# Optimization experiments

Hardware: AMD Instinct MI355X
Metric: run time of the kernel (lower is better)

The kernel has to match this reference:

```python
import jax, jax.numpy as jnp
import numpy as np
from jax import lax

C = 256      # in_c == out_c == dim
NH = 8       # num_heads
K = 7        # depthwise pos-enc kernel
H1 = 512     # int(mlp_ratio * in_c) = 2.0 * 256
B, Hs, Ws = 2, 48, 48


def setup_inputs() -> dict:
    key = jax.random.key(0)
    ks = jax.random.split(key, 8)
    w = lambda k, shape: jax.random.normal(k, shape, jnp.float32) * 0.02
    return {
        "x": jax.random.normal(ks[0], (B, C, Hs, Ws), jnp.float32),
        # 1x1 convs stored as [out, in] (BN folded into weight+bias)
        "qk_w": w(ks[1], (2 * C, C)), "qk_b": jnp.zeros((2 * C,), jnp.float32),
        "v_w": w(ks[2], (C, C)),       "v_b": jnp.zeros((C,), jnp.float32),
        # depthwise positional encoding conv [C,1,K,K]
        "pe_w": w(ks[3], (C, 1, K, K)), "pe_b": jnp.zeros((C,), jnp.float32),
        "proj_w": w(ks[4], (C, C)),    "proj_b": jnp.zeros((C,), jnp.float32),
        # conv FFN: 1x1 (SiLU) -> 1x1 (no act)
        "fc1_w": w(ks[5], (H1, C)),    "fc1_b": jnp.zeros((H1,), jnp.float32),
        "fc2_w": w(ks[6], (C, H1)),    "fc2_b": jnp.zeros((C,), jnp.float32),
    }


def _c1(x, w, b):
    # 1x1 conv == per-pixel matmul
    return jnp.einsum('bchw,oc->bohw', x, w) + b[None, :, None, None]


def reference(x, qk_w, qk_b, v_w, v_b, pe_w, pe_b, proj_w, proj_b,
              fc1_w, fc1_b, fc2_w, fc2_b):
    Bb, Cc, Hh, Ww = x.shape
    hd = Cc // NH                 # head_dim = 32
    N = Hh * Ww
    scale = hd ** -0.5

    # ---- AttentionV2 ----
    qk = _c1(x, qk_w, qk_b).reshape(Bb, NH, 2 * hd, N)
    q, k = qk[:, :, :hd], qk[:, :, hd:]
    v_full = _c1(x, v_w, v_b)                      # [B,C,H,W]
    pe = lax.conv_general_dilated(
        v_full, pe_w, (1, 1), 'SAME', feature_group_count=Cc,
        dimension_numbers=('NCHW', 'OIHW', 'NCHW')) + pe_b[None, :, None, None]
    v = v_full.reshape(Bb, NH, hd, N)

    # attn = q^T @ k * scale ; softmax over keys
    attn = jax.nn.softmax(jnp.einsum('bhdn,bhdm->bhnm', q, k) * scale, axis=-1)
    o = jnp.einsum('bhdm,bhnm->bhdn', v, attn).reshape(Bb, Cc, Hh, Ww)
    attn_out = _c1(o + pe, proj_w, proj_b)

    # ---- block residuals + conv FFN (add=True) ----
    x1 = x + attn_out
    h = jax.nn.silu(_c1(x1, fc1_w, fc1_b))         # Conv(in_c, hidden, 1, 1) with SiLU
    return x1 + _c1(h, fc2_w, fc2_b)               # Conv(hidden, out_c, 1, act=False)
```

## Files before the change

### kernel.cpp

```cpp
#include <hip/hip_runtime.h>
#include <hip/hip_bf16.h>

#define NCH 256
#define NHD 8
#define HD 32
#define NPIX 2304
#define H1DIM 512

typedef __attribute__((ext_vector_type(8))) __bf16 bf16x8;
typedef __attribute__((ext_vector_type(4))) float f32x4;

__global__ __launch_bounds__(256) void prep_k(
    const float* __restrict__ x,
    const float* __restrict__ w0, const float* __restrict__ w1,
    const float* __restrict__ w2, const float* __restrict__ w3,
    const float* __restrict__ w4,
    __bf16* __restrict__ Xb, __bf16* __restrict__ Wall) {
    const int tid = threadIdx.x;
    if (blockIdx.x < 288) {
        const int t = blockIdx.x;
        const int b = t / 144, r0 = t % 144;
        const int c0 = (r0 / 36) * 64, n0 = (r0 % 36) * 64;
        __shared__ float tile[64][65];
        const size_t sb = ((size_t)b * NCH + c0) * NPIX + n0;
#pragma unroll
        for (int i = 0; i < 16; ++i) {
            int idx = tid + i * 256;
            int rr = idx >> 6, cc = idx & 63;
            tile[rr][cc] = x[sb + (size_t)rr * NPIX + cc];
        }
        __syncthreads();
#pragma unroll
        for (int i = 0; i < 8; ++i) {
            int idx = tid + i * 256;
            int nn = idx >> 5, cp = (idx & 31) * 2;
            union { __bf16 h[2]; unsigned u; } pk;
            pk.h[0] = (__bf16)tile[cp][nn];
            pk.h[1] = (__bf16)tile[cp + 1][nn];
            *(unsigned*)&Xb[((size_t)b * NPIX + n0 + nn) * NCH + c0 + cp] = pk.u;
        }
    } else {
        int i = (blockIdx.x - 288) * 256 + tid;
        const float* src; int off;
        if (i < 32768)      { src = w0; off = i; }
        else if (i < 49152) { src = w1; off = i - 32768; }
        else if (i < 65536) { src = w2; off = i - 49152; }
        else if (i < 98304) { src = w3; off = i - 65536; }
        else                { src = w4; off = i - 98304; }
        float4 v = ((const float4*)src)[off];
        union { __bf16 h[4]; uint2 u; } pk;
        pk.h[0] = (__bf16)v.x; pk.h[1] = (__bf16)v.y;
        pk.h[2] = (__bf16)v.z; pk.h[3] = (__bf16)v.w;
        ((uint2*)Wall)[i] = pk.u;
    }
}

__global__ __launch_bounds__(256) void qkv_k(
    const __bf16* __restrict__ A, const __bf16* __restrict__ Wq,
    const __bf16* __restrict__ Wv, const float* __restrict__ qk_b,
    const float* __restrict__ v_b, __bf16* __restrict__ Qb,
    __bf16* __restrict__ Kf, float* __restrict__ v_bu,
    __bf16* __restrict__ Vf) {
    const int tid = threadIdx.x;
    const int wave = tid >> 6, lane = tid & 63;
    const int l16 = lane & 15, quad = lane >> 4;
    const int h = blockIdx.x & 7;
    const int u = blockIdx.x >> 3;
    const int tau = u * 4 + wave;
    const int px = tau % 144;
    const int rest = tau / 144;
    const int b = rest & 1;
    const int sub = rest >> 1;
    const int m0 = px * 16;
    const bool isv = sub >= 4;
    const int oc0 = isv ? (32 * h + 16 * (sub - 4)) : (64 * h + 16 * sub);
    const __bf16* W = isv ? Wv : Wq;

    const __bf16* aptr = A + ((size_t)b * NPIX + m0 + l16) * NCH + quad * 8;
    const __bf16* bptr = W + (size_t)(oc0 + l16) * NCH + quad * 8;

    f32x4 acc = {0.f, 0.f, 0.f, 0.f};
#pragma unroll 8
    for (int k = 0; k < NCH; k += 32) {
        bf16x8 af = *(const bf16x8*)(aptr + k);
        bf16x8 bf = *(const bf16x8*)(bptr + k);
        acc = __builtin_amdgcn_mfma_f32_16x16x32_bf16(af, bf, acc, 0, 0, 0);
    }

    const int oc = oc0 + l16;
    const int mb = m0 + quad * 4;

    if (!isv) {
        const float bb = qk_b[oc];
        const int bh = b * NHD + h;
        const int dd = (oc0 & 16) + l16;
        if ((oc0 & 32) == 0) {
            const float qs = 0.17677669529663689f * 1.4426950408889634f;
#pragma unroll
            for (int r = 0; r < 4; ++r)
                Qb[((size_t)bh * NPIX + mb + r) * 32 + dd] = (__bf16)((acc[r] + bb) * qs);
        } else {
            __bf16* kp = Kf + ((size_t)(bh * 144 + px) * 64 + (dd >> 3) * 16 + quad * 4) * 8 + (dd & 7);
#pragma unroll
            for (int r = 0; r < 4; ++r) kp[r * 8] = (__bf16)(acc[r] + bb);
        }
    } else {
        const float bb = v_b[oc];
        const int bh = b * NHD + h;
        const int half = (oc0 >> 4) & 1;
        const size_t fb = ((size_t)b * NCH + oc) * NPIX + mb;
        float4 vf_; float* vp = &vf_.x;
        union { __bf16 hh[4]; uint2 u; } pk;
#pragma unroll
        for (int r = 0; r < 4; ++r) {
            float v = acc[r] + bb;
            vp[r] = v; pk.hh[r] = (__bf16)v;
        }
        *(float4*)&v_bu[fb] = vf_;
        *(uint2*)&Vf[((size_t)(bh * 144 + px) * 64 + lane) * 8 + half * 4] = pk.u;
    }
}

template <int IC, int OC, int OCQ, int MODE>
__global__ __launch_bounds__(256) void convmm_k(
    const __bf16* __restrict__ A, const __bf16* __restrict__ W,
    const float* __restrict__ bias, const float* __restrict__ resid,
    float* __restrict__ out_f, __bf16* __restrict__ out_b) {
    const int tid = threadIdx.x;
    const int wave = tid >> 6, lane = tid & 63;
    const int l16 = lane & 15, quad = lane >> 4;
    const int xcd = blockIdx.x & 7;
    const int u = blockIdx.x >> 3;
    const int ocq = u % OCQ;
    const int rest = u / OCQ;
    const int m8 = rest % 18;
    const int b = rest / 18;
    const int m0 = (m8 * 8 + xcd) * 16;
    const int oc0 = (ocq * 4 + wave) * 16;

    const __bf16* aptr = A + ((size_t)b * NPIX + m0 + l16) * IC + quad * 8;
    const __bf16* bptr = W + (size_t)(oc0 + l16) * IC + quad * 8;

    f32x4 acc = {0.f, 0.f, 0.f, 0.f};
#pragma unroll 8
    for (int k = 0; k < IC; k += 32) {
        bf16x8 af = *(const bf16x8*)(aptr + k);
        bf16x8 bf = *(const bf16x8*)(bptr + k);
        acc = __builtin_amdgcn_mfma_f32_16x16x32_bf16(af, bf, acc, 0, 0, 0);
    }

    const int oc = oc0 + l16;
    const int mb = m0 + quad * 4;
    const float bb = bias[oc];

    if constexpr (MODE == 2) {
        const size_t fb = ((size_t)b * OC + oc) * NPIX + mb;
        float4 xr = *(const float4*)&resid[fb];
        const float* xp = &xr.x;
        float4 vf_; float* vp = &vf_.x;
#pragma unroll
        for (int r = 0; r < 4; ++r) {
            float v = acc[r] + bb + xp[r];
            vp[r] = v;
            out_b[((size_t)b * NPIX + mb + r) * OC + oc] = (__bf16)v;
        }
        *(float4*)&out_f[fb] = vf_;
    } else if constexpr (MODE == 3) {
#pragma unroll
        for (int r = 0; r < 4; ++r) {
            float v = acc[r] + bb;
            v = v / (1.f + __expf(-v));
            out_b[((size_t)b * NPIX + mb + r) * OC + oc] = (__bf16)v;
        }
    } else {
        const size_t fb = ((size_t)b * OC + oc) * NPIX + mb;
        float4 xr = *(const float4*)&resid[fb];
        const float* xp = &xr.x;
        float4 vf_; float* vp = &vf_.x;
#pragma unroll
        for (int r = 0; r < 4; ++r) vp[r] = acc[r] + bb + xp[r];
        *(float4*)&out_f[fb] = vf_;
    }
}

__global__ __launch_bounds__(256) void dwconv_k(const float* __restrict__ vb,
                                                const float* __restrict__ pw,
                                                const float* __restrict__ pb,
                                                float* __restrict__ pe) {
    const int tid = threadIdx.x;
    const int r = (int)blockIdx.x >> 3;
    const int c = (blockIdx.x & 7) * 32 + (r & 31);
    const int b = r >> 5;
    __shared__ float plane[NPIX];
    __shared__ float wk[49];
    const size_t base = ((size_t)b * NCH + c) * NPIX;
    for (int i = tid; i < NPIX; i += 256) plane[i] = vb[base + i];
    if (tid < 49) wk[tid] = pw[c * 49 + tid];
    float bb = pb[c];
    __syncthreads();
    for (int p = tid; p < NPIX; p += 256) {
        int y = p / 48, x = p - y * 48;
        float s = bb;
#pragma unroll
        for (int ky = 0; ky < 7; ++ky) {
            int yy = y + ky - 3;
            if ((unsigned)yy < 48u) {
#pragma unroll
                for (int kx = 0; kx < 7; ++kx) {
                    int xx = x + kx - 3;
                    if ((unsigned)xx < 48u) s += wk[ky * 7 + kx] * plane[yy * 48 + xx];
                }
            }
        }
        pe[base + p] = s;
    }
}

__global__ __launch_bounds__(512) void attn6_k(const __bf16* __restrict__ Qb,
                                               const __bf16* __restrict__ Kf,
                                               const __bf16* __restrict__ Vf,
                                               const float* __restrict__ pe,
                                               __bf16* __restrict__ opb) {
    const int tid = threadIdx.x;
    const int wave = tid >> 6, lane = tid & 63;
    const int l16 = lane & 15, quad = lane >> 4;
    const int h = blockIdx.x & 7;
    const int r0 = (int)blockIdx.x >> 3;
    const int qt = r0 % 72;
    const int b = r0 / 72;
    const int qb = qt * 32;
    const int bh = b * NHD + h;

    __shared__ float o_s[8][32][33];
    __shared__ float l_s[8][32];

    bf16x8 b_q0 = *(const bf16x8*)(Qb + ((size_t)bh * NPIX + qb + l16) * 32 + quad * 8);
    bf16x8 b_q1 = *(const bf16x8*)(Qb + ((size_t)bh * NPIX + qb + 16 + l16) * 32 + quad * 8);

    const __bf16* kf = Kf + ((size_t)(bh * 144 + wave * 18) * 64 + lane) * 8;
    const __bf16* vf = Vf + ((size_t)(bh * 144 + wave * 18) * 64 + lane) * 8;

    f32x4 o00 = {0.f,0.f,0.f,0.f}, o01 = {0.f,0.f,0.f,0.f};
    f32x4 o10 = {0.f,0.f,0.f,0.f}, o11 = {0.f,0.f,0.f,0.f};
    f32x4 l0 = {0.f,0.f,0.f,0.f}, l1 = {0.f,0.f,0.f,0.f};

#pragma unroll 3
    for (int t = 0; t < 18; ++t) {
        bf16x8 a_k = *(const bf16x8*)(kf + (size_t)t * 512);
        bf16x8 va  = *(const bf16x8*)(vf + (size_t)t * 512);
        f32x4 z = {0.f, 0.f, 0.f, 0.f};
        f32x4 s0 = __builtin_amdgcn_mfma_f32_16x16x32_bf16(a_k, b_q0, z, 0, 0, 0);
        f32x4 s1 = __builtin_amdgcn_mfma_f32_16x16x32_bf16(a_k, b_q1, z, 0, 0, 0);
        f32x4 p0, p1;
#pragma unroll
        for (int r = 0; r < 4; ++r) {
            p0[r] = __builtin_amdgcn_exp2f(s0[r]);
            p1[r] = __builtin_amdgcn_exp2f(s1[r]);
        }
        l0 += p0; l1 += p1;
        bf16x8 b0lo = {}, b0hi = {}, b1lo = {}, b1hi = {};
#pragma unroll
        for (int r = 0; r < 4; ++r) {
            __bf16 c0 = (__bf16)p0[r], c1 = (__bf16)p1[r];
            b0lo[r] = c0; b0hi[4 + r] = c0;
            b1lo[r] = c1; b1hi[4 + r] = c1;
        }
        o00 = __builtin_amdgcn_mfma_f32_16x16x32_bf16(va, b0lo, o00, 0, 0, 0);
        o01 = __builtin_amdgcn_mfma_f32_16x16x32_bf16(va, b0hi, o01, 0, 0, 0);
        o10 = __builtin_amdgcn_mfma_f32_16x16x32_bf16(va, b1lo, o10, 0, 0, 0);
        o11 = __builtin_amdgcn_mfma_f32_16x16x32_bf16(va, b1hi, o11, 0, 0, 0);
    }

    float ls0 = l0[0] + l0[1] + l0[2] + l0[3];
    ls0 += __shfl_xor(ls0, 16); ls0 += __shfl_xor(ls0, 32);
    float ls1 = l1[0] + l1[1] + l1[2] + l1[3];
    ls1 += __shfl_xor(ls1, 16); ls1 += __shfl_xor(ls1, 32);

#pragma unroll
    for (int r = 0; r < 4; ++r) {
        o_s[wave][quad * 4 + r][l16]           = o00[r];
        o_s[wave][16 + quad * 4 + r][l16]      = o01[r];
        o_s[wave][quad * 4 + r][16 + l16]      = o10[r];
        o_s[wave][16 + quad * 4 + r][16 + l16] = o11[r];
    }
    if (quad == 0) { l_s[wave][l16] = ls0; l_s[wave][16 + l16] = ls1; }
    __syncthreads();

    const int q = tid & 31;
    const int d0 = (tid >> 5) * 2;
    float l = 0.f;
#pragma unroll
    for (int w = 0; w < 8; ++w) l += l_s[w][q];
    const float inv = 1.f / l;
    float v0 = 0.f, v1 = 0.f;
#pragma unroll
    for (int w = 0; w < 8; ++w) {
        v0 += o_s[w][d0][q];
        v1 += o_s[w][d0 + 1][q];
    }
    const int n = qb + q;
    const int ch = h * HD + d0;
    v0 = v0 * inv + pe[((size_t)b * NCH + ch) * NPIX + n];
    v1 = v1 * inv + pe[((size_t)b * NCH + ch + 1) * NPIX + n];
    union { __bf16 hh[2]; unsigned u; } pk;
    pk.hh[0] = (__bf16)v0; pk.hh[1] = (__bf16)v1;
    *(unsigned*)&opb[((size_t)b * NPIX + n) * NCH + ch] = pk.u;
}

extern "C" void kernel_launch(void* const* d_in, const int* in_sizes, int n_in,
                              void* d_out, int out_size, void* d_ws, size_t ws_size,
                              hipStream_t stream) {
    const float* x    = (const float*)d_in[0];
    const float* qk_w = (const float*)d_in[1];
    const float* qk_b = (const float*)d_in[2];
    const float* v_w  = (const float*)d_in[3];
    const float* v_b  = (const float*)d_in[4];
    const float* pe_w = (const float*)d_in[5];
    const float* pe_b = (const float*)d_in[6];
    const float* pj_w = (const float*)d_in[7];
    const float* pj_b = (const float*)d_in[8];
    const float* f1_w = (const float*)d_in[9];
    const float* f1_b = (const float*)d_in[10];
    const float* f2_w = (const float*)d_in[11];
    const float* f2_b = (const float*)d_in[12];
    float* out = (float*)d_out;

    const int B = 2;
    const size_t plane = (size_t)NCH * NPIX;
    const size_t bp = (size_t)B * plane;

    float* v_bu  = (float*)d_ws;
    float* pe_bu = v_bu + bp;
    float* x1_f  = pe_bu + bp;
    __bf16* Xb   = (__bf16*)(x1_f + bp);
    __bf16* opb  = Xb + bp;
    __bf16* x1b  = opb + bp;
    __bf16* hb   = x1b + bp;
    __bf16* Qb   = hb + 2 * bp;
    __bf16* Kf   = Qb + bp;
    __bf16* Vf   = Kf + bp;
    __bf16* Wall = Vf + bp;
    __bf16* Wq = Wall;
    __bf16* Wv = Wall + 131072;
    __bf16* Wp = Wall + 196608;
    __bf16* W1 = Wall + 262144;
    __bf16* W2 = Wall + 393216;

    prep_k<<<800, 256, 0, stream>>>(x, qk_w, v_w, pj_w, f1_w, f2_w, Xb, Wall);
    qkv_k<<<3456, 256, 0, stream>>>(Xb, Wq, Wv, qk_b, v_b, Qb, Kf, v_bu, Vf);
    dwconv_k<<<512, 256, 0, stream>>>(v_bu, pe_w, pe_b, pe_bu);
    attn6_k<<<1152, 512, 0, stream>>>(Qb, Kf, Vf, pe_bu, opb);
    convmm_k<256, 256, 4, 2><<<1152, 256, 0, stream>>>(opb, Wp, pj_b, x, x1_f, x1b);
    convmm_k<256, 512, 8, 3><<<2304, 256, 0, stream>>>(x1b, W1, f1_b, nullptr, nullptr, hb);
    convmm_k<512, 256, 4, 4><<<1152, 256, 0, stream>>>(hb, W2, f2_b, x1_f, out, nullptr);
}
```

Measured before the change: 208.3 us.

## Fuse all seven stages into one persistent cooperative kernel with grid syncs

Replaces the seven separate kernel launches (prep, qkv, dwconv, attention, three 1x1 convs) with a single persistent cooperative kernel. Blocks loop over each stage's tasks and are separated by grid.sync barriers. The grid size comes from an occupancy query capped at 1024 blocks. This removes per-launch overhead and inter-kernel gaps, but adds grid-wide barrier costs. Occupancy may also drop because of the larger union shared memory and register pressure across all stages.

```diff
diff --git a/kernel.cpp b/kernel.cpp
--- a/kernel.cpp
+++ b/kernel.cpp
@@ -1,142 +1,41 @@
 #include <hip/hip_runtime.h>
 #include <hip/hip_bf16.h>
+#include <hip/hip_cooperative_groups.h>
+
+namespace cg = cooperative_groups;
 
 #define NCH 256
 #define NHD 8
 #define HD 32
 #define NPIX 2304
 #define H1DIM 512
+#define NCU 256
 
 typedef __attribute__((ext_vector_type(8))) __bf16 bf16x8;
 typedef __attribute__((ext_vector_type(4))) float f32x4;
 
-__global__ __launch_bounds__(256) void prep_k(
-    const float* __restrict__ x,
-    const float* __restrict__ w0, const float* __restrict__ w1,
-    const float* __restrict__ w2, const float* __restrict__ w3,
-    const float* __restrict__ w4,
-    __bf16* __restrict__ Xb, __bf16* __restrict__ Wall) {
-    const int tid = threadIdx.x;
-    if (blockIdx.x < 288) {
-        const int t = blockIdx.x;
-        const int b = t / 144, r0 = t % 144;
-        const int c0 = (r0 / 36) * 64, n0 = (r0 % 36) * 64;
-        __shared__ float tile[64][65];
-        const size_t sb = ((size_t)b * NCH + c0) * NPIX + n0;
-#pragma unroll
-        for (int i = 0; i < 16; ++i) {
-            int idx = tid + i * 256;
-            int rr = idx >> 6, cc = idx & 63;
-            tile[rr][cc] = x[sb + (size_t)rr * NPIX + cc];
-        }
-        __syncthreads();
-#pragma unroll
-        for (int i = 0; i < 8; ++i) {
-            int idx = tid + i * 256;
-            int nn = idx >> 5, cp = (idx & 31) * 2;
-            union { __bf16 h[2]; unsigned u; } pk;
-            pk.h[0] = (__bf16)tile[cp][nn];
-            pk.h[1] = (__bf16)tile[cp + 1][nn];
-            *(unsigned*)&Xb[((size_t)b * NPIX + n0 + nn) * NCH + c0 + cp] = pk.u;
-        }
-    } else {
-        int i = (blockIdx.x - 288) * 256 + tid;
-        const float* src; int off;
-        if (i < 32768)      { src = w0; off = i; }
-        else if (i < 49152) { src = w1; off = i - 32768; }
-        else if (i < 65536) { src = w2; off = i - 49152; }
-        else if (i < 98304) { src = w3; off = i - 65536; }
-        else                { src = w4; off = i - 98304; }
-        float4 v = ((const float4*)src)[off];
-        union { __bf16 h[4]; uint2 u; } pk;
-        pk.h[0] = (__bf16)v.x; pk.h[1] = (__bf16)v.y;
-        pk.h[2] = (__bf16)v.z; pk.h[3] = (__bf16)v.w;
-        ((uint2*)Wall)[i] = pk.u;
-    }
-}
-
-__global__ __launch_bounds__(256) void qkv_k(
-    const __bf16* __restrict__ A, const __bf16* __restrict__ Wq,
-    const __bf16* __restrict__ Wv, const float* __restrict__ qk_b,
-    const float* __restrict__ v_b, __bf16* __restrict__ Qb,
-    __bf16* __restrict__ Kf, float* __restrict__ v_bu,
-    __bf16* __restrict__ Vf) {
-    const int tid = threadIdx.x;
-    const int wave = tid >> 6, lane = tid & 63;
-    const int l16 = lane & 15, quad = lane >> 4;
-    const int h = blockIdx.x & 7;
-    const int u = blockIdx.x >> 3;
-    const int tau = u * 4 + wave;
-    const int px = tau % 144;
-    const int rest = tau / 144;
-    const int b = rest & 1;
-    const int sub = rest >> 1;
-    const int m0 = px * 16;
-    const bool isv = sub >= 4;
-    const int oc0 = isv ? (32 * h + 16 * (sub - 4)) : (64 * h + 16 * sub);
-    const __bf16* W = isv ? Wv : Wq;
-
-    const __bf16* aptr = A + ((size_t)b * NPIX + m0 + l16) * NCH + quad * 8;
-    const __bf16* bptr = W + (size_t)(oc0 + l16) * NCH + quad * 8;
-
-    f32x4 acc = {0.f, 0.f, 0.f, 0.f};
-#pragma unroll 8
-    for (int k = 0; k < NCH; k += 32) {
-        bf16x8 af = *(const bf16x8*)(aptr + k);
-        bf16x8 bf = *(const bf16x8*)(bptr + k);
-        acc = __builtin_amdgcn_mfma_f32_16x16x32_bf16(af, bf, acc, 0, 0, 0);
-    }
-
-    const int oc = oc0 + l16;
-    const int mb = m0 + quad * 4;
-
-    if (!isv) {
-        const float bb = qk_b[oc];
-        const int bh = b * NHD + h;
-        const int dd = (oc0 & 16) + l16;
-        if ((oc0 & 32) == 0) {
-            const float qs = 0.17677669529663689f * 1.4426950408889634f;
-#pragma unroll
-            for (int r = 0; r < 4; ++r)
-                Qb[((size_t)bh * NPIX + mb + r) * 32 + dd] = (__bf16)((acc[r] + bb) * qs);
-        } else {
-            __bf16* kp = Kf + ((size_t)(bh * 144 + px) * 64 + (dd >> 3) * 16 + quad * 4) * 8 + (dd & 7);
-#pragma unroll
-            for (int r = 0; r < 4; ++r) kp[r * 8] = (__bf16)(acc[r] + bb);
-        }
-    } else {
-        const float bb = v_b[oc];
-        const int bh = b * NHD + h;
-        const int half = (oc0 >> 4) & 1;
-        const size_t fb = ((size_t)b * NCH + oc) * NPIX + mb;
-        float4 vf_; float* vp = &vf_.x;
-        union { __bf16 hh[4]; uint2 u; } pk;
-#pragma unroll
-        for (int r = 0; r < 4; ++r) {
-            float v = acc[r] + bb;
-            vp[r] = v; pk.hh[r] = (__bf16)v;
-        }
-        *(float4*)&v_bu[fb] = vf_;
-        *(uint2*)&Vf[((size_t)(bh * 144 + px) * 64 + lane) * 8 + half * 4] = pk.u;
-    }
-}
+union SMem {
+    float tile[64][65];
+    struct { float plane[NPIX]; float wk[64]; } dw;
+    struct { float o[8][32][33]; float l[8][32]; } at;
+};
 
 template <int IC, int OC, int OCQ, int MODE>
-__global__ __launch_bounds__(256) void convmm_k(
-    const __bf16* __restrict__ A, const __bf16* __restrict__ W,
+__device__ __forceinline__ void convmm_task(
+    int T, const __bf16* __restrict__ A, const __bf16* __restrict__ W,
     const float* __restrict__ bias, const float* __restrict__ resid,
-    float* __restrict__ out_f, __bf16* __restrict__ out_b) {
-    const int tid = threadIdx.x;
-    const int wave = tid >> 6, lane = tid & 63;
-    const int l16 = lane & 15, quad = lane >> 4;
-    const int xcd = blockIdx.x & 7;
-    const int u = blockIdx.x >> 3;
+    float* __restrict__ out_f, __bf16* __restrict__ out_b,
+    int l16, int quad) {
+    const int w4 = T & 3;
+    const int obid = T >> 2;
+    const int xcd = obid & 7;
+    const int u = obid >> 3;
     const int ocq = u % OCQ;
     const int rest = u / OCQ;
     const int m8 = rest % 18;
     const int b = rest / 18;
     const int m0 = (m8 * 8 + xcd) * 16;
-    const int oc0 = (ocq * 4 + wave) * 16;
+    const int oc0 = (ocq * 4 + w4) * 16;
 
     const __bf16* aptr = A + ((size_t)b * NPIX + m0 + l16) * IC + quad * 8;
     const __bf16* bptr = W + (size_t)(oc0 + l16) * IC + quad * 8;
@@ -183,128 +82,250 @@
     }
 }
 
-__global__ __launch_bounds__(256) void dwconv_k(const float* __restrict__ vb,
-                                                const float* __restrict__ pw,
-                                                const float* __restrict__ pb,
-                                                float* __restrict__ pe) {
-    const int tid = threadIdx.x;
-    const int r = (int)blockIdx.x >> 3;
-    const int c = (blockIdx.x & 7) * 32 + (r & 31);
-    const int b = r >> 5;
-    __shared__ float plane[NPIX];
-    __shared__ float wk[49];
-    const size_t base = ((size_t)b * NCH + c) * NPIX;
-    for (int i = tid; i < NPIX; i += 256) plane[i] = vb[base + i];
-    if (tid < 49) wk[tid] = pw[c * 49 + tid];
-    float bb = pb[c];
-    __syncthreads();
-    for (int p = tid; p < NPIX; p += 256) {
-        int y = p / 48, x = p - y * 48;
-        float s = bb;
-#pragma unroll
-        for (int ky = 0; ky < 7; ++ky) {
-            int yy = y + ky - 3;
-            if ((unsigned)yy < 48u) {
-#pragma unroll
-                for (int kx = 0; kx < 7; ++kx) {
-                    int xx = x + kx - 3;
-                    if ((unsigned)xx < 48u) s += wk[ky * 7 + kx] * plane[yy * 48 + xx];
-                }
-            }
-        }
-        pe[base + p] = s;
-    }
-}
-
-__global__ __launch_bounds__(512) void attn6_k(const __bf16* __restrict__ Qb,
-                                               const __bf16* __restrict__ Kf,
-                                               const __bf16* __restrict__ Vf,
-                                               const float* __restrict__ pe,
-                                               __bf16* __restrict__ opb) {
+__global__ __launch_bounds__(512, 4) void fused_k(
+    const float* __restrict__ x, const float* __restrict__ qk_w,
+    const float* __restrict__ v_w, const float* __restrict__ pj_w,
+    const float* __restrict__ f1_w, const float* __restrict__ f2_w,
+    const float* __restrict__ qk_b, const float* __restrict__ v_b,
+    const float* __restrict__ pe_w, const float* __restrict__ pe_b,
+    const float* __restrict__ pj_b, const float* __restrict__ f1_b,
+    const float* __restrict__ f2_b,
+    float* __restrict__ out, float* __restrict__ v_bu,
+    float* __restrict__ pe_bu, float* __restrict__ x1_f,
+    __bf16* __restrict__ Xb, __bf16* __restrict__ opb,
+    __bf16* __restrict__ x1b, __bf16* __restrict__ hb,
+    __bf16* __restrict__ Qb, __bf16* __restrict__ Kf,
+    __bf16* __restrict__ Vf, __bf16* __restrict__ Wall) {
+    cg::grid_group grid = cg::this_grid();
     const int tid = threadIdx.x;
     const int wave = tid >> 6, lane = tid & 63;
     const int l16 = lane & 15, quad = lane >> 4;
-    const int h = blockIdx.x & 7;
-    const int r0 = (int)blockIdx.x >> 3;
-    const int qt = r0 % 72;
-    const int b = r0 / 72;
-    const int qb = qt * 32;
-    const int bh = b * NHD + h;
-
-    __shared__ float o_s[8][32][33];
-    __shared__ float l_s[8][32];
-
-    bf16x8 b_q0 = *(const bf16x8*)(Qb + ((size_t)bh * NPIX + qb + l16) * 32 + quad * 8);
-    bf16x8 b_q1 = *(const bf16x8*)(Qb + ((size_t)bh * NPIX + qb + 16 + l16) * 32 + quad * 8);
-
-    const __bf16* kf = Kf + ((size_t)(bh * 144 + wave * 18) * 64 + lane) * 8;
-    const __bf16* vf = Vf + ((size_t)(bh * 144 + wave * 18) * 64 + lane) * 8;
-
-    f32x4 o00 = {0.f,0.f,0.f,0.f}, o01 = {0.f,0.f,0.f,0.f};
-    f32x4 o10 = {0.f,0.f,0.f,0.f}, o11 = {0.f,0.f,0.f,0.f};
-    f32x4 l0 = {0.f,0.f,0.f,0.f}, l1 = {0.f,0.f,0.f,0.f};
+    const int bid = (int)blockIdx.x;
+    const int nb = (int)gridDim.x;
+
+    __shared__ SMem sm;
+
+    const __bf16* Wq = Wall;
+    const __bf16* Wv = Wall + 131072;
+    const __bf16* Wp = Wall + 196608;
+    const __bf16* W1 = Wall + 262144;
+    const __bf16* W2 = Wall + 393216;
+
+    for (int t = bid; t < 288; t += nb) {
+        const int b = t / 144, r0 = t % 144;
+        const int c0 = (r0 / 36) * 64, n0 = (r0 % 36) * 64;
+        const size_t sb = ((size_t)b * NCH + c0) * NPIX + n0;
+        for (int i = tid; i < 4096; i += 512) {
+            int rr = i >> 6, cc = i & 63;
+            sm.tile[rr][cc] = x[sb + (size_t)rr * NPIX + cc];
+        }
+        __syncthreads();
+        for (int i = tid; i < 2048; i += 512) {
+            int nn = i >> 5, cp = (i & 31) * 2;
+            union { __bf16 h[2]; unsigned u; } pk;
+            pk.h[0] = (__bf16)sm.tile[cp][nn];
+            pk.h[1] = (__bf16)sm.tile[cp + 1][nn];
+            *(unsigned*)&Xb[((size_t)b * NPIX + n0 + nn) * NCH + c0 + cp] = pk.u;
+        }
+        __syncthreads();
+    }
+    for (int i = bid * 512 + tid; i < 131072; i += nb * 512) {
+        const float* src; int off;
+        if (i < 32768)      { src = qk_w; off = i; }
+        else if (i < 49152) { src = v_w;  off = i - 32768; }
+        else if (i < 65536) { src = pj_w; off = i - 49152; }
+        else if (i < 98304) { src = f1_w; off = i - 65536; }
+        else                { src = f2_w; off = i - 98304; }
+        float4 v = ((const float4*)src)[off];
+        union { __bf16 h[4]; uint2 u; } pk;
+        pk.h[0] = (__bf16)v.x; pk.h[1] = (__bf16)v.y;
+        pk.h[2] = (__bf16)v.z; pk.h[3] = (__bf16)v.w;
+        ((uint2*)Wall)[i] = pk.u;
+    }
+    grid.sync();
+
+    {
+        const int h = bid & 7;
+        const int slots = (nb >> 3) * 8;
+        for (int tau = (bid >> 3) * 8 + wave; tau < 1728; tau += slots) {
+            const int px = tau % 144;
+            const int rest = tau / 144;
+            const int b = rest & 1;
+            const int sub = rest >> 1;
+            const int m0 = px * 16;
+            const bool isv = sub >= 4;
+            const int oc0 = isv ? (32 * h + 16 * (sub - 4)) : (64 * h + 16 * sub);
+            const __bf16* W = isv ? Wv : Wq;
+
+            const __bf16* aptr = Xb + ((size_t)b * NPIX + m0 + l16) * NCH + quad * 8;
+            const __bf16* bptr = W + (size_t)(oc0 + l16) * NCH + quad * 8;
+
+            f32x4 acc = {0.f, 0.f, 0.f, 0.f};
+#pragma unroll 8
+            for (int k = 0; k < NCH; k += 32) {
+                bf16x8 af = *(const bf16x8*)(aptr + k);
+                bf16x8 bf = *(const bf16x8*)(bptr + k);
+                acc = __builtin_amdgcn_mfma_f32_16x16x32_bf16(af, bf, acc, 0, 0, 0);
+            }
+
+            const int oc = oc0 + l16;
+            const int mb = m0 + quad * 4;
+
+            if (!isv) {
+                const float bb = qk_b[oc];
+                const int bh = b * NHD + h;
+                const int dd = (oc0 & 16) + l16;
+                if ((oc0 & 32) == 0) {
+                    const float qs = 0.17677669529663689f * 1.4426950408889634f;
+#pragma unroll
+                    for (int r = 0; r < 4; ++r)
+                        Qb[((size_t)bh * NPIX + mb + r) * 32 + dd] = (__bf16)((acc[r] + bb) * qs);
+                } else {
+                    __bf16* kp = Kf + ((size_t)(bh * 144 + px) * 64 + (dd >> 3) * 16 + quad * 4) * 8 + (dd & 7);
+#pragma unroll
+                    for (int r = 0; r < 4; ++r) kp[r * 8] = (__bf16)(acc[r] + bb);
+                }
+            } else {
+                const float bb = v_b[oc];
+                const int bh = b * NHD + h;
+                const int half = (oc0 >> 4) & 1;
+                const size_t fb = ((size_t)b * NCH + oc) * NPIX + mb;
+                float4 vf_; float* vp = &vf_.x;
+                union { __bf16 hh[4]; uint2 u; } pk;
+#pragma unroll
+                for (int r = 0; r < 4; ++r) {
+                    float v = acc[r] + bb;
+                    vp[r] = v; pk.hh[r] = (__bf16)v;
+                }
+                *(float4*)&v_bu[fb] = vf_;
+                *(uint2*)&Vf[((size_t)(bh * 144 + px) * 64 + lane) * 8 + half * 4] = pk.u;
+            }
+        }
+    }
+    grid.sync();
+
+    for (int t = bid; t < 512; t += nb) {
+        const int r = t >> 3;
+        const int c = (t & 7) * 32 + (r & 31);
+        const int b = r >> 5;
+        const size_t base = ((size_t)b * NCH + c) * NPIX;
+        for (int i = tid; i < NPIX; i += 512) sm.dw.plane[i] = v_bu[base + i];
+        if (tid < 49) sm.dw.wk[tid] = pe_w[c * 49 + tid];
+        const float bb = pe_b[c];
+        __syncthreads();
+        for (int p = tid; p < NPIX; p += 512) {
+            int y = p / 48, xx0 = p - y * 48;
+            float s = bb;
+#pragma unroll
+            for (int ky = 0; ky < 7; ++ky) {
+                int yy = y + ky - 3;
+                if ((unsigned)yy < 48u) {
+#pragma unroll
+                    for (int kx = 0; kx < 7; ++kx) {
+                        int xx = xx0 + kx - 3;
+                        if ((unsigned)xx < 48u) s += sm.dw.wk[ky * 7 + kx] * sm.dw.plane[yy * 48 + xx];
+                    }
+                }
+            }
+            pe_bu[base + p] = s;
+        }
+        __syncthreads();
+    }
+    grid.sync();
+
+    for (int task = bid; task < 1152; task += nb) {
+        const int h = task & 7;
+        const int r0 = task >> 3;
+        const int qt = r0 % 72;
+        const int b = r0 / 72;
+        const int qb = qt * 32;
+        const int bh = b * NHD + h;
+
+        bf16x8 b_q0 = *(const bf16x8*)(Qb + ((size_t)bh * NPIX + qb + l16) * 32 + quad * 8);
+        bf16x8 b_q1 = *(const bf16x8*)(Qb + ((size_t)bh * NPIX + qb + 16 + l16) * 32 + quad * 8);
+
+        const __bf16* kf = Kf + ((size_t)(bh * 144 + wave * 18) * 64 + lane) * 8;
+        const __bf16* vf = Vf + ((size_t)(bh * 144 + wave * 18) * 64 + lane) * 8;
+
+        f32x4 o00 = {0.f,0.f,0.f,0.f}, o01 = {0.f,0.f,0.f,0.f};
+        f32x4 o10 = {0.f,0.f,0.f,0.f}, o11 = {0.f,0.f,0.f,0.f};
+        f32x4 l0 = {0.f,0.f,0.f,0.f}, l1 = {0.f,0.f,0.f,0.f};
 
 #pragma unroll 3
-    for (int t = 0; t < 18; ++t) {
-        bf16x8 a_k = *(const bf16x8*)(kf + (size_t)t * 512);
-        bf16x8 va  = *(const bf16x8*)(vf + (size_t)t * 512);
-        f32x4 z = {0.f, 0.f, 0.f, 0.f};
-        f32x4 s0 = __builtin_amdgcn_mfma_f32_16x16x32_bf16(a_k, b_q0, z, 0, 0, 0);
-        f32x4 s1 = __builtin_amdgcn_mfma_f32_16x16x32_bf16(a_k, b_q1, z, 0, 0, 0);
-        f32x4 p0, p1;
+        for (int t = 0; t < 18; ++t) {
+            bf16x8 a_k = *(const bf16x8*)(kf + (size_t)t * 512);
+            bf16x8 va  = *(const bf16x8*)(vf + (size_t)t * 512);
+            f32x4 z = {0.f, 0.f, 0.f, 0.f};
+            f32x4 s0 = __builtin_amdgcn_mfma_f32_16x16x32_bf16(a_k, b_q0, z, 0, 0, 0);
+            f32x4 s1 = __builtin_amdgcn_mfma_f32_16x16x32_bf16(a_k, b_q1, z, 0, 0, 0);
+            f32x4 p0, p1;
+#pragma unroll
+            for (int r = 0; r < 4; ++r) {
+                p0[r] = __builtin_amdgcn_exp2f(s0[r]);
+                p1[r] = __builtin_amdgcn_exp2f(s1[r]);
+            }
+            l0 += p0; l1 += p1;
+            bf16x8 b0lo = {}, b0hi = {}, b1lo = {}, b1hi = {};
+#pragma unroll
+            for (int r = 0; r < 4; ++r) {
+                __bf16 c0 = (__bf16)p0[r], c1 = (__bf16)p1[r];
+                b0lo[r] = c0; b0hi[4 + r] = c0;
+                b1lo[r] = c1; b1hi[4 + r] = c1;
+            }
+            o00 = __builtin_amdgcn_mfma_f32_16x16x32_bf16(va, b0lo, o00, 0, 0, 0);
+            o01 = __builtin_amdgcn_mfma_f32_16x16x32_bf16(va, b0hi, o01, 0, 0, 0);
+            o10 = __builtin_amdgcn_mfma_f32_16x16x32_bf16(va, b1lo, o10, 0, 0, 0);
+            o11 = __builtin_amdgcn_mfma_f32_16x16x32_bf16(va, b1hi, o11, 0, 0, 0);
+        }
+
+        float ls0 = l0[0] + l0[1] + l0[2] + l0[3];
+        ls0 += __shfl_xor(ls0, 16); ls0 += __shfl_xor(ls0, 32);
+        float ls1 = l1[0] + l1[1] + l1[2] + l1[3];
+        ls1 += __shfl_xor(ls1, 16); ls1 += __shfl_xor(ls1, 32);
+
 #pragma unroll
         for (int r = 0; r < 4; ++r) {
-            p0[r] = __builtin_amdgcn_exp2f(s0[r]);
-            p1[r] = __builtin_amdgcn_exp2f(s1[r]);
-        }
-        l0 += p0; l1 += p1;
-        bf16x8 b0lo = {}, b0hi = {}, b1lo = {}, b1hi = {};
-#pragma unroll
-        for (int r = 0; r < 4; ++r) {
-            __bf16 c0 = (__bf16)p0[r], c1 = (__bf16)p1[r];
-            b0lo[r] = c0; b0hi[4 + r] = c0;
-            b1lo[r] = c1; b1hi[4 + r] = c1;
-        }
-        o00 = __builtin_amdgcn_mfma_f32_16x16x32_bf16(va, b0lo, o00, 0, 0, 0);
-        o01 = __builtin_amdgcn_mfma_f32_16x16x32_bf16(va, b0hi, o01, 0, 0, 0);
-        o10 = __builtin_amdgcn_mfma_f32_16x16x32_bf16(va, b1lo, o10, 0, 0, 0);
-        o11 = __builtin_amdgcn_mfma_f32_16x16x32_bf16(va, b1hi, o11, 0, 0, 0);
-    }
-
-    float ls0 = l0[0] + l0[1] + l0[2] + l0[3];
-    ls0 += __shfl_xor(ls0, 16); ls0 += __shfl_xor(ls0, 32);
-    float ls1 = l1[0] + l1[1] + l1[2] + l1[3];
-    ls1 += __shfl_xor(ls1, 16); ls1 += __shfl_xor(ls1, 32);
-
-#pragma unroll
-    for (int r = 0; r < 4; ++r) {
-        o_s[wave][quad * 4 + r][l16]           = o00[r];
-        o_s[wave][16 + quad * 4 + r][l16]      = o01[r];
-        o_s[wave][quad * 4 + r][16 + l16]      = o10[r];
-        o_s[wave][16 + quad * 4 + r][16 + l16] = o11[r];
-    }
-    if (quad == 0) { l_s[wave][l16] = ls0; l_s[wave][16 + l16] = ls1; }
-    __syncthreads();
-
-    const int q = tid & 31;
-    const int d0 = (tid >> 5) * 2;
-    float l = 0.f;
-#pragma unroll
-    for (int w = 0; w < 8; ++w) l += l_s[w][q];
-    const float inv = 1.f / l;
-    float v0 = 0.f, v1 = 0.f;
-#pragma unroll
-    for (int w = 0; w < 8; ++w) {
-        v0 += o_s[w][d0][q];
-        v1 += o_s[w][d0 + 1][q];
-    }
-    const int n = qb + q;
-    const int ch = h * HD + d0;
-    v0 = v0 * inv + pe[((size_t)b * NCH + ch) * NPIX + n];
-    v1 = v1 * inv + pe[((size_t)b * NCH + ch + 1) * NPIX + n];
-    union { __bf16 hh[2]; unsigned u; } pk;
-    pk.hh[0] = (__bf16)v0; pk.hh[1] = (__bf16)v1;
-    *(unsigned*)&opb[((size_t)b * NPIX + n) * NCH + ch] = pk.u;
+            sm.at.o[wave][quad * 4 + r][l16]           = o00[r];
+            sm.at.o[wave][16 + quad * 4 + r][l16]      = o01[r];
+            sm.at.o[wave][quad * 4 + r][16 + l16]      = o10[r];
+            sm.at.o[wave][16 + quad * 4 + r][16 + l16] = o11[r];
+        }
+        if (quad == 0) { sm.at.l[wave][l16] = ls0; sm.at.l[wave][16 + l16] = ls1; }
+        __syncthreads();
+
+        const int q = tid & 31;
+        const int d0 = (tid >> 5) * 2;
+        float l = 0.f;
+#pragma unroll
+        for (int w = 0; w < 8; ++w) l += sm.at.l[w][q];
+        const float inv = 1.f / l;
+        float v0 = 0.f, v1 = 0.f;
+#pragma unroll
+        for (int w = 0; w < 8; ++w) {
+            v0 += sm.at.o[w][d0][q];
+            v1 += sm.at.o[w][d0 + 1][q];
+        }
+        const int n = qb + q;
+        const int ch = h * HD + d0;
+        v0 = v0 * inv + pe_bu[((size_t)b * NCH + ch) * NPIX + n];
+        v1 = v1 * inv + pe_bu[((size_t)b * NCH + ch + 1) * NPIX + n];
+        union { __bf16 hh[2]; unsigned u; } pk;
+        pk.hh[0] = (__bf16)v0; pk.hh[1] = (__bf16)v1;
+        *(unsigned*)&opb[((size_t)b * NPIX + n) * NCH + ch] = pk.u;
+        __syncthreads();
+    }
+    grid.sync();
+
+    for (int T = bid * 8 + wave; T < 4608; T += nb * 8)
+        convmm_task<256, 256, 4, 2>(T, opb, Wp, pj_b, x, x1_f, x1b, l16, quad);
+    grid.sync();
+
+    for (int T = bid * 8 + wave; T < 9216; T += nb * 8)
+        convmm_task<256, 512, 8, 3>(T, x1b, W1, f1_b, nullptr, nullptr, hb, l16, quad);
+    grid.sync();
+
+    for (int T = bid * 8 + wave; T < 4608; T += nb * 8)
+        convmm_task<512, 256, 4, 4>(T, hb, W2, f2_b, x1_f, out, nullptr, l16, quad);
 }
 
 extern "C" void kernel_launch(void* const* d_in, const int* in_sizes, int n_in,
@@ -340,17 +361,24 @@
     __bf16* Kf   = Qb + bp;
     __bf16* Vf   = Kf + bp;
     __bf16* Wall = Vf + bp;
-    __bf16* Wq = Wall;
-    __bf16* Wv = Wall + 131072;
-    __bf16* Wp = Wall + 196608;
-    __bf16* W1 = Wall + 262144;
-    __bf16* W2 = Wall + 393216;
-
-    prep_k<<<800, 256, 0, stream>>>(x, qk_w, v_w, pj_w, f1_w, f2_w, Xb, Wall);
-    qkv_k<<<3456, 256, 0, stream>>>(Xb, Wq, Wv, qk_b, v_b, Qb, Kf, v_bu, Vf);
-    dwconv_k<<<512, 256, 0, stream>>>(v_bu, pe_w, pe_b, pe_bu);
-    attn6_k<<<1152, 512, 0, stream>>>(Qb, Kf, Vf, pe_bu, opb);
-    convmm_k<256, 256, 4, 2><<<1152, 256, 0, stream>>>(opb, Wp, pj_b, x, x1_f, x1b);
-    convmm_k<256, 512, 8, 3><<<2304, 256, 0, stream>>>(x1b, W1, f1_b, nullptr, nullptr, hb);
-    convmm_k<512, 256, 4, 4><<<1152, 256, 0, stream>>>(hb, W2, f2_b, x1_f, out, nullptr);
+
+    static int nblk = 0;
+    if (nblk == 0) {
+        int occ = 0;
+        hipOccupancyMaxActiveBlocksPerMultiprocessor(&occ, fused_k, 512, 0);
+        if (occ < 1) occ = 1;
+        long g = (long)occ * NCU;
+        if (g > 1024) g = 1024;
+        g &= ~7L;
+        if (g < 8) g = 8;
+        nblk = (int)g;
+    }
+
+    void* ka[] = {
+        (void*)&x,    (void*)&qk_w, (void*)&v_w,  (void*)&pj_w, (void*)&f1_w,
+        (void*)&f2_w, (void*)&qk_b, (void*)&v_b,  (void*)&pe_w, (void*)&pe_b,
+        (void*)&pj_b, (void*)&f1_b, (void*)&f2_b, (void*)&out,  (void*)&v_bu,
+        (void*)&pe_bu,(void*)&x1_f, (void*)&Xb,   (void*)&opb,  (void*)&x1b,
+        (void*)&hb,   (void*)&Qb,   (void*)&Kf,   (void*)&Vf,   (void*)&Wall};
+    hipLaunchCooperativeKernel(fused_k, dim3(nblk), dim3(512), ka, 0, stream);
 }
```

Measured after the change: 417.3 us. 2x slower.

## Fuse projection, FFN fc1 and fc2 into one kernel with LDS intermediates

Applied to the files above, without the earlier changes.

Replaces the three separate 1x1-conv GEMM launches (proj+residual, fc1+SiLU, fc2+residual) with one kernel. Each block handles 16 pixels and keeps x1 and the hidden activations in shared memory. This removes global writes and reads of the x1 and hidden buffers and two kernel launches. In exchange the grid shrinks to 288 blocks, which lowers parallelism, and each block re-reads all weights from global or L2.

```diff
diff --git a/kernel.cpp b/kernel.cpp
--- a/kernel.cpp
+++ b/kernel.cpp
@@ -121,68 +121,6 @@
     }
 }
 
-template <int IC, int OC, int OCQ, int MODE>
-__global__ __launch_bounds__(256) void convmm_k(
-    const __bf16* __restrict__ A, const __bf16* __restrict__ W,
-    const float* __restrict__ bias, const float* __restrict__ resid,
-    float* __restrict__ out_f, __bf16* __restrict__ out_b) {
-    const int tid = threadIdx.x;
-    const int wave = tid >> 6, lane = tid & 63;
-    const int l16 = lane & 15, quad = lane >> 4;
-    const int xcd = blockIdx.x & 7;
-    const int u = blockIdx.x >> 3;
-    const int ocq = u % OCQ;
-    const int rest = u / OCQ;
-    const int m8 = rest % 18;
-    const int b = rest / 18;
-    const int m0 = (m8 * 8 + xcd) * 16;
-    const int oc0 = (ocq * 4 + wave) * 16;
-
-    const __bf16* aptr = A + ((size_t)b * NPIX + m0 + l16) * IC + quad * 8;
-    const __bf16* bptr = W + (size_t)(oc0 + l16) * IC + quad * 8;
-
-    f32x4 acc = {0.f, 0.f, 0.f, 0.f};
-#pragma unroll 8
-    for (int k = 0; k < IC; k += 32) {
-        bf16x8 af = *(const bf16x8*)(aptr + k);
-        bf16x8 bf = *(const bf16x8*)(bptr + k);
-        acc = __builtin_amdgcn_mfma_f32_16x16x32_bf16(af, bf, acc, 0, 0, 0);
-    }
-
-    const int oc = oc0 + l16;
-    const int mb = m0 + quad * 4;
-    const float bb = bias[oc];
-
-    if constexpr (MODE == 2) {
-        const size_t fb = ((size_t)b * OC + oc) * NPIX + mb;
-        float4 xr = *(const float4*)&resid[fb];
-        const float* xp = &xr.x;
-        float4 vf_; float* vp = &vf_.x;
-#pragma unroll
-        for (int r = 0; r < 4; ++r) {
-            float v = acc[r] + bb + xp[r];
-            vp[r] = v;
-            out_b[((size_t)b * NPIX + mb + r) * OC + oc] = (__bf16)v;
-        }
-        *(float4*)&out_f[fb] = vf_;
-    } else if constexpr (MODE == 3) {
-#pragma unroll
-        for (int r = 0; r < 4; ++r) {
-            float v = acc[r] + bb;
-            v = v / (1.f + __expf(-v));
-            out_b[((size_t)b * NPIX + mb + r) * OC + oc] = (__bf16)v;
-        }
-    } else {
-        const size_t fb = ((size_t)b * OC + oc) * NPIX + mb;
-        float4 xr = *(const float4*)&resid[fb];
-        const float* xp = &xr.x;
-        float4 vf_; float* vp = &vf_.x;
-#pragma unroll
-        for (int r = 0; r < 4; ++r) vp[r] = acc[r] + bb + xp[r];
-        *(float4*)&out_f[fb] = vf_;
-    }
-}
-
 __global__ __launch_bounds__(256) void dwconv_k(const float* __restrict__ vb,
                                                 const float* __restrict__ pw,
                                                 const float* __restrict__ pb,
@@ -305,6 +243,89 @@
     union { __bf16 hh[2]; unsigned u; } pk;
     pk.hh[0] = (__bf16)v0; pk.hh[1] = (__bf16)v1;
     *(unsigned*)&opb[((size_t)b * NPIX + n) * NCH + ch] = pk.u;
+}
+
+__global__ __launch_bounds__(512) void mlp_k(
+    const __bf16* __restrict__ opb, const __bf16* __restrict__ Wp,
+    const __bf16* __restrict__ W1, const __bf16* __restrict__ W2,
+    const float* __restrict__ pj_b, const float* __restrict__ f1_b,
+    const float* __restrict__ f2_b, const float* __restrict__ x,
+    float* __restrict__ out) {
+    const int tid = threadIdx.x;
+    const int wave = tid >> 6, lane = tid & 63;
+    const int l16 = lane & 15, quad = lane >> 4;
+    const int b = (int)blockIdx.x / 144;
+    const int m0 = ((int)blockIdx.x % 144) * 16;
+
+    __shared__ __bf16 x1h[16][264];
+    __shared__ float  x1f[16][260];
+    __shared__ __bf16 hh[16][520];
+
+#pragma unroll
+    for (int t = 0; t < 2; ++t) {
+        const int oc0 = (wave + t * 8) * 16;
+        const __bf16* aptr = opb + ((size_t)b * NPIX + m0 + l16) * NCH + quad * 8;
+        const __bf16* bptr = Wp + (size_t)(oc0 + l16) * NCH + quad * 8;
+        f32x4 acc = {0.f, 0.f, 0.f, 0.f};
+#pragma unroll 8
+        for (int k = 0; k < NCH; k += 32) {
+            bf16x8 af = *(const bf16x8*)(aptr + k);
+            bf16x8 bf = *(const bf16x8*)(bptr + k);
+            acc = __builtin_amdgcn_mfma_f32_16x16x32_bf16(af, bf, acc, 0, 0, 0);
+        }
+        const int oc = oc0 + l16;
+        const float bb = pj_b[oc];
+        float4 xr = *(const float4*)&x[((size_t)b * NCH + oc) * NPIX + m0 + quad * 4];
+        const float* xp = &xr.x;
+#pragma unroll
+        for (int r = 0; r < 4; ++r) {
+            float v = acc[r] + bb + xp[r];
+            x1f[quad * 4 + r][oc] = v;
+            x1h[quad * 4 + r][oc] = (__bf16)v;
+        }
+    }
+    __syncthreads();
+
+#pragma unroll
+    for (int t = 0; t < 4; ++t) {
+        const int oc0 = (wave + t * 8) * 16;
+        const __bf16* bptr = W1 + (size_t)(oc0 + l16) * NCH + quad * 8;
+        f32x4 acc = {0.f, 0.f, 0.f, 0.f};
+#pragma unroll 8
+        for (int k = 0; k < NCH; k += 32) {
+            bf16x8 af = *(const bf16x8*)&x1h[l16][quad * 8 + k];
+            bf16x8 bf = *(const bf16x8*)(bptr + k);
+            acc = __builtin_amdgcn_mfma_f32_16x16x32_bf16(af, bf, acc, 0, 0, 0);
+        }
+        const int oc = oc0 + l16;
+        const float bb = f1_b[oc];
+#pragma unroll
+        for (int r = 0; r < 4; ++r) {
+            float v = acc[r] + bb;
+            v = v / (1.f + __expf(-v));
+            hh[quad * 4 + r][oc] = (__bf16)v;
+        }
+    }
+    __syncthreads();
+
+#pragma unroll
+    for (int t = 0; t < 2; ++t) {
+        const int oc0 = (wave + t * 8) * 16;
+        const __bf16* bptr = W2 + (size_t)(oc0 + l16) * H1DIM + quad * 8;
+        f32x4 acc = {0.f, 0.f, 0.f, 0.f};
+#pragma unroll 8
+        for (int k = 0; k < H1DIM; k += 32) {
+            bf16x8 af = *(const bf16x8*)&hh[l16][quad * 8 + k];
+            bf16x8 bf = *(const bf16x8*)(bptr + k);
+            acc = __builtin_amdgcn_mfma_f32_16x16x32_bf16(af, bf, acc, 0, 0, 0);
+        }
+        const int oc = oc0 + l16;
+        const float bb = f2_b[oc];
+        float4 vf_; float* vp = &vf_.x;
+#pragma unroll
+        for (int r = 0; r < 4; ++r) vp[r] = acc[r] + bb + x1f[quad * 4 + r][oc];
+        *(float4*)&out[((size_t)b * NCH + oc) * NPIX + m0 + quad * 4] = vf_;
+    }
 }
 
 extern "C" void kernel_launch(void* const* d_in, const int* in_sizes, int n_in,
@@ -331,12 +352,9 @@
 
     float* v_bu  = (float*)d_ws;
     float* pe_bu = v_bu + bp;
-    float* x1_f  = pe_bu + bp;
-    __bf16* Xb   = (__bf16*)(x1_f + bp);
+    __bf16* Xb   = (__bf16*)(pe_bu + bp);
     __bf16* opb  = Xb + bp;
-    __bf16* x1b  = opb + bp;
-    __bf16* hb   = x1b + bp;
-    __bf16* Qb   = hb + 2 * bp;
+    __bf16* Qb   = opb + bp;
     __bf16* Kf   = Qb + bp;
     __bf16* Vf   = Kf + bp;
     __bf16* Wall = Vf + bp;
@@ -350,7 +368,5 @@
     qkv_k<<<3456, 256, 0, stream>>>(Xb, Wq, Wv, qk_b, v_b, Qb, Kf, v_bu, Vf);
     dwconv_k<<<512, 256, 0, stream>>>(v_bu, pe_w, pe_b, pe_bu);
     attn6_k<<<1152, 512, 0, stream>>>(Qb, Kf, Vf, pe_bu, opb);
-    convmm_k<256, 256, 4, 2><<<1152, 256, 0, stream>>>(opb, Wp, pj_b, x, x1_f, x1b);
-    convmm_k<256, 512, 8, 3><<<2304, 256, 0, stream>>>(x1b, W1, f1_b, nullptr, nullptr, hb);
-    convmm_k<512, 256, 4, 4><<<1152, 256, 0, stream>>>(hb, W2, f2_b, x1_f, out, nullptr);
-}
+    mlp_k<<<288, 512, 0, stream>>>(opb, Wp, W1, W2, pj_b, f1_b, f2_b, x, out);
+}
```

New measurement: 199.5 us. 4.2% less time.
